# Kernel tuning notes

Measured on AMD Instinct MI355X. Metric: run time of the kernel, lower is better.

Reference implementation:

```python
import jax, jax.numpy as jnp
import numpy as np

B, D, H = 2048, 1024, 16
DH = D // H            # 64 head dim
R = DH // 2            # 32 random-feature dim (kernel_type has no 'northogonal')
EPS = 1e-3             # keras LayerNormalization default epsilon


def _orthogonal(seed):
    # mirrors random_orthogonal(shape=(1,H,1,DH,R)): QR of flat (H*DH, R) matrix
    rng = np.random.default_rng(seed)
    a = rng.standard_normal((H * DH, R)).astype(np.float32)
    q, r = np.linalg.qr(a)
    q = q * np.sign(np.diag(r))[None, :]
    return jnp.asarray(q.reshape(H, DH, R))


def setup_inputs() -> dict:
    key = jax.random.key(0)
    ks = jax.random.split(key, 8)
    inp = {
        "x": jax.random.normal(ks[0], (B, D), jnp.float32),
        # states start as small positive values so den = phi4(q) . new_z > 0
        "s": jax.random.uniform(ks[1], (B, D * R), jnp.float32),
        "z": jax.random.uniform(ks[2], (B, R * H), jnp.float32),
        "ln1_g": jnp.ones((D,), jnp.float32),
        "ln1_b": jnp.zeros((D,), jnp.float32),
        "ln2_g": jnp.ones((D,), jnp.float32),
        "ln2_b": jnp.zeros((D,), jnp.float32),
        "W_attn": jax.random.normal(ks[3], (D, 3 * D), jnp.float32) * 0.02,
        "b_attn": jnp.zeros((3 * D,), jnp.float32),
        "W_proj": jax.random.normal(ks[4], (D, D), jnp.float32) * 0.02,
        "b_proj": jnp.zeros((D,), jnp.float32),
        "W_fc": jax.random.normal(ks[5], (D, 4 * D), jnp.float32) * 0.02,
        "b_fc": jnp.zeros((4 * D,), jnp.float32),
        "W_mp": jax.random.normal(ks[6], (4 * D, D), jnp.float32) * 0.02,
        "b_mp": jnp.zeros((D,), jnp.float32),
    }
    for i in range(4):
        inp[f"w{i + 1}"] = _orthogonal(100 + i)
    return inp


def _ln(x, g, b):
    m = jnp.mean(x, axis=-1, keepdims=True)
    v = jnp.var(x, axis=-1, keepdims=True)
    return g * (x - m) * jax.lax.rsqrt(v + EPS) + b


def _phi(x, w):
    # x: [B,H,dh], w: [H,dh,R] orthogonal random features; kernel 'sigmoid'
    return jax.nn.sigmoid(jnp.einsum('bhd,hdr->bhr', x, w))


def reference(x, s, z, ln1_g, ln1_b, ln2_g, ln2_b, W_attn, b_attn,
              W_proj, b_proj, W_fc, b_fc, W_mp, b_mp, w1, w2, w3, w4):
    bsz = x.shape[0]
    h1 = _ln(x, ln1_g, ln1_b)
    qkv = h1 @ W_attn + b_attn                      # [B, 3D]
    q, k, v = jnp.split(qkv, 3, axis=1)
    q = q.reshape(bsz, H, DH)
    k = k.reshape(bsz, H, DH)
    v = v.reshape(bsz, H, DH)
    s4 = s.reshape(bsz, H, R, DH)
    z3 = z.reshape(bsz, H, R)
    # kernelized linear-attention state update (outer-product accumulation)
    new_s = s4 + jnp.einsum('bhr,bhd->bhrd', _phi(k, w1), v)   # [B,H,R,DH]
    new_z = z3 + _phi(k, w2)                                   # [B,H,R]
    num = jnp.einsum('bhr,bhrd->bhd', _phi(q, w3), new_s)      # [B,H,DH]
    den = jnp.einsum('bhr,bhr->bh', _phi(q, w4), new_z)[..., None]
    head = (num / den).reshape(bsz, D)
    attention = head @ W_proj + b_proj
    h2 = _ln(attention + x, ln2_g, ln2_b)          # dropout: inference mode
    ffn = jax.nn.gelu(h2 @ W_fc + b_fc, approximate=False) @ W_mp + b_mp
    out = h2 + ffn
    return out, new_s.reshape(bsz, D * R), new_z.reshape(bsz, R * H)
```

## Files before the change

### kernel.cpp

```cpp
#include <hip/hip_runtime.h>
#include <hip/hip_bf16.h>
#include <math.h>


#define Bsz 2048
#define Dm  1024
#define Hh  16
#define DHd 64
#define Rr  32

typedef __bf16 bf16x8 __attribute__((ext_vector_type(8)));
typedef float  f32x4  __attribute__((ext_vector_type(4)));

__device__ __forceinline__ float bf2f(__bf16 x) { return (float)x; }
__device__ __forceinline__ __bf16 f2bf(float x) { return (__bf16)x; }

template<bool ADD, typename TA>
__global__ __launch_bounds__(256) void ln_kernel(
    const TA* __restrict__ a, const float* __restrict__ b2,
    const float* __restrict__ g, const float* __restrict__ beta,
    __bf16* __restrict__ outb, float* __restrict__ outf)
{
  const int row = blockIdx.x;
  const int t = threadIdx.x;
  const size_t base = (size_t)row * Dm;
  float vals[4];
#pragma unroll
  for (int i = 0; i < 4; ++i) {
    const int c = t * 4 + i;
    float v = (float)a[base + c];
    if (ADD) v += b2[base + c];
    vals[i] = v;
  }
  float sm = 0.f, sq = 0.f;
#pragma unroll
  for (int i = 0; i < 4; ++i) { sm += vals[i]; sq += vals[i] * vals[i]; }
  for (int off = 32; off > 0; off >>= 1) {
    sm += __shfl_down(sm, off);
    sq += __shfl_down(sq, off);
  }
  __shared__ float smw[4], sqw[4];
  if ((t & 63) == 0) { smw[t >> 6] = sm; sqw[t >> 6] = sq; }
  __syncthreads();
  const float S  = smw[0] + smw[1] + smw[2] + smw[3];
  const float SS = sqw[0] + sqw[1] + sqw[2] + sqw[3];
  const float mean = S * (1.f / Dm);
  const float var  = SS * (1.f / Dm) - mean * mean;
  const float inv  = rsqrtf(var + 1e-3f);
#pragma unroll
  for (int i = 0; i < 4; ++i) {
    const int c = t * 4 + i;
    const float r = g[c] * ((vals[i] - mean) * inv) + beta[c];
    outb[base + c] = f2bf(r);
    if (ADD) outf[base + c] = r;
  }
}

template<bool GELU, bool RES, bool OUTF32>
__global__ __launch_bounds__(256) void gemm_kernel(
    const __bf16* __restrict__ A, const float* __restrict__ B,
    const float* __restrict__ bias, const float* __restrict__ res,
    void* __restrict__ Cv, int M, int N, int K)
{
  __shared__ __align__(16) __bf16 lsA[64][40];
  __shared__ __align__(16) __bf16 lsB[64][40];
  const int t = threadIdx.x;
  const int wave = t >> 6, lane = t & 63;
  const int quad = lane >> 4, l16 = lane & 15;
  const int bm = blockIdx.x * 64, bn = blockIdx.y * 64;
  f32x4 acc0 = {0.f, 0.f, 0.f, 0.f};
  f32x4 acc1 = {0.f, 0.f, 0.f, 0.f};
  f32x4 acc2 = {0.f, 0.f, 0.f, 0.f};
  f32x4 acc3 = {0.f, 0.f, 0.f, 0.f};
  const int arow = t >> 2, acol = (t & 3) * 8;
  const int bncol = t & 63, bkrow = (t >> 6) * 8;
  const size_t abase = (size_t)(bm + arow) * K + acol;

  for (int kt = 0; kt < K; kt += 32) {
    uint4 av = *(const uint4*)(A + abase + kt);
    *(uint4*)(&lsA[arow][acol]) = av;
#pragma unroll
    for (int j = 0; j < 8; ++j)
      lsB[bncol][bkrow + j] = f2bf(B[(size_t)(kt + bkrow + j) * N + bn + bncol]);
    __syncthreads();
    bf16x8 af  = *(const bf16x8*)(&lsA[wave * 16 + l16][quad * 8]);
    bf16x8 bf0 = *(const bf16x8*)(&lsB[      l16][quad * 8]);
    bf16x8 bf1 = *(const bf16x8*)(&lsB[16 + l16][quad * 8]);
    bf16x8 bf2 = *(const bf16x8*)(&lsB[32 + l16][quad * 8]);
    bf16x8 bf3 = *(const bf16x8*)(&lsB[48 + l16][quad * 8]);
    acc0 = __builtin_amdgcn_mfma_f32_16x16x32_bf16(af, bf0, acc0, 0, 0, 0);
    acc1 = __builtin_amdgcn_mfma_f32_16x16x32_bf16(af, bf1, acc1, 0, 0, 0);
    acc2 = __builtin_amdgcn_mfma_f32_16x16x32_bf16(af, bf2, acc2, 0, 0, 0);
    acc3 = __builtin_amdgcn_mfma_f32_16x16x32_bf16(af, bf3, acc3, 0, 0, 0);
    __syncthreads();
  }

  const int m0 = bm + wave * 16 + quad * 4;
  f32x4 accs[4] = {acc0, acc1, acc2, acc3};
#pragma unroll
  for (int ns = 0; ns < 4; ++ns) {
    const int col = bn + ns * 16 + l16;
    const float bv = bias[col];
#pragma unroll
    for (int i = 0; i < 4; ++i) {
      const int row = m0 + i;
      float v = accs[ns][i] + bv;
      if (GELU) v = 0.5f * v * (1.0f + erff(v * 0.70710678118654752f));
      if (RES) v += res[(size_t)row * N + col];
      if (OUTF32) ((float*)Cv)[(size_t)row * N + col] = v;
      else        ((__bf16*)Cv)[(size_t)row * N + col] = f2bf(v);
    }
  }
}

__global__ __launch_bounds__(64) void attn_kernel(
    const float* __restrict__ qkv, const float* __restrict__ s,
    const float* __restrict__ z,
    const float* __restrict__ w1, const float* __restrict__ w2,
    const float* __restrict__ w3, const float* __restrict__ w4,
    float* __restrict__ new_s, float* __restrict__ new_z,
    __bf16* __restrict__ head)
{
  const int bh = blockIdx.x;
  const int b = bh >> 4, h = bh & 15;
  const int tid = threadIdx.x;
  __shared__ float ksh[64], qsh[64];
  __shared__ float phish[4][32];
  __shared__ float nzsh[32];

  const float* qrow = qkv + (size_t)b * (3 * Dm);
  const float qv = qrow[h * 64 + tid];
  const float kv = qrow[Dm + h * 64 + tid];
  const float vv = qrow[2 * Dm + h * 64 + tid];
  qsh[tid] = qv; ksh[tid] = kv;
  __syncthreads();

  {
    const int r = tid & 31;
    const float* wm[4] = {w1, w2, w3, w4};
    for (int mm = (tid >> 5); mm < 4; mm += 2) {
      const float* w = wm[mm] + (size_t)h * (DHd * Rr) + r;
      const float* src = (mm < 2) ? ksh : qsh;
      float acc = 0.f;
#pragma unroll 8
      for (int d = 0; d < 64; ++d) acc += src[d] * w[(size_t)d * 32];
      phish[mm][r] = 1.f / (1.f + expf(-acc));
    }
  }
  __syncthreads();

  const size_t zbase = (size_t)b * (Rr * Hh) + h * Rr;
  if (tid < 32) {
    const float nz = z[zbase + tid] + phish[1][tid];
    new_z[zbase + tid] = nz;
    nzsh[tid] = nz;
  }
  __syncthreads();

  float den = 0.f;
#pragma unroll
  for (int r = 0; r < 32; ++r) den += phish[3][r] * nzsh[r];

  const size_t sbase = ((size_t)b * Hh + h) * (Rr * DHd);
  float num = 0.f;
#pragma unroll 4
  for (int r = 0; r < 32; ++r) {
    const float ns = s[sbase + r * 64 + tid] + phish[0][r] * vv;
    new_s[sbase + r * 64 + tid] = ns;
    num += phish[2][r] * ns;
  }
  head[(size_t)b * Dm + h * 64 + tid] = f2bf(num / den);
}

extern "C" void kernel_launch(void* const* d_in, const int* in_sizes, int n_in,
                              void* d_out, int out_size, void* d_ws, size_t ws_size,
                              hipStream_t stream)
{
  const float* x      = (const float*)d_in[0];
  const float* s_in   = (const float*)d_in[1];
  const float* z_in   = (const float*)d_in[2];
  const float* ln1_g  = (const float*)d_in[3];
  const float* ln1_b  = (const float*)d_in[4];
  const float* ln2_g  = (const float*)d_in[5];
  const float* ln2_b  = (const float*)d_in[6];
  const float* W_attn = (const float*)d_in[7];
  const float* b_attn = (const float*)d_in[8];
  const float* W_proj = (const float*)d_in[9];
  const float* b_proj = (const float*)d_in[10];
  const float* W_fc   = (const float*)d_in[11];
  const float* b_fc   = (const float*)d_in[12];
  const float* W_mp   = (const float*)d_in[13];
  const float* b_mp   = (const float*)d_in[14];
  const float* w1     = (const float*)d_in[15];
  const float* w2     = (const float*)d_in[16];
  const float* w3     = (const float*)d_in[17];
  const float* w4     = (const float*)d_in[18];

  float* out0  = (float*)d_out;
  float* out_s = out0 + (size_t)Bsz * Dm;
  float* out_z = out_s + (size_t)Bsz * Dm * Rr;

  char* ws = (char*)d_ws;
  __bf16* h1    = (__bf16*)ws; ws += (size_t)Bsz * Dm * 2;
  float*  qkv   = (float*) ws; ws += (size_t)Bsz * 3 * Dm * 4;
  __bf16* headp = (__bf16*)ws; ws += (size_t)Bsz * Dm * 2;
  __bf16* attnb = (__bf16*)ws; ws += (size_t)Bsz * Dm * 2;
  __bf16* h2b   = (__bf16*)ws; ws += (size_t)Bsz * Dm * 2;
  float*  h2f   = (float*) ws; ws += (size_t)Bsz * Dm * 4;
  __bf16* fcb   = (__bf16*)ws; ws += (size_t)Bsz * 4 * Dm * 2;

  ln_kernel<false, float><<<Bsz, 256, 0, stream>>>(
      x, nullptr, ln1_g, ln1_b, h1, nullptr);
  gemm_kernel<false, false, true><<<dim3(Bsz / 64, (3 * Dm) / 64), 256, 0, stream>>>(
      h1, W_attn, b_attn, nullptr, qkv, Bsz, 3 * Dm, Dm);
  attn_kernel<<<Bsz * Hh, 64, 0, stream>>>(qkv, s_in, z_in, w1, w2, w3, w4,
                                           out_s, out_z, headp);
  gemm_kernel<false, false, false><<<dim3(Bsz / 64, Dm / 64), 256, 0, stream>>>(
      headp, W_proj, b_proj, nullptr, attnb, Bsz, Dm, Dm);
  ln_kernel<true, __bf16><<<Bsz, 256, 0, stream>>>(
      attnb, x, ln2_g, ln2_b, h2b, h2f);
  gemm_kernel<true, false, false><<<dim3(Bsz / 64, (4 * Dm) / 64), 256, 0, stream>>>(
      h2b, W_fc, b_fc, nullptr, fcb, Bsz, 4 * Dm, Dm);
  gemm_kernel<false, true, true><<<dim3(Bsz / 64, Dm / 64), 256, 0, stream>>>(
      fcb, W_mp, b_mp, h2f, out0, Bsz, Dm, 4 * Dm);
}
```

Before: 803.9 us.

## Pre-transpose weights to bf16 and load GEMM tiles via global_load_lds

Adds a transpose kernel that converts each fp32 weight matrix to a K-contiguous bf16 copy in workspace, run each call. The GEMM then streams both A and B tiles straight into LDS with 16-byte global_load_lds instead of strided scalar fp32 loads plus conversion. Tiles are generalized to BM×BN with a 2x2 wave layout, using 64x128 for the wide QKV and FC GEMMs. Workspace regions are reused by lifetime to fit the weight copies, at the cost of extra transpose launches and traffic on every call.

```diff
diff --git a/kernel.cpp b/kernel.cpp
--- a/kernel.cpp
+++ b/kernel.cpp
@@ -12,8 +12,30 @@
 typedef __bf16 bf16x8 __attribute__((ext_vector_type(8)));
 typedef float  f32x4  __attribute__((ext_vector_type(4)));
 
-__device__ __forceinline__ float bf2f(__bf16 x) { return (float)x; }
 __device__ __forceinline__ __bf16 f2bf(float x) { return (__bf16)x; }
+
+#define GLOAD_LDS16(g, l) __builtin_amdgcn_global_load_lds(               \
+    (const __attribute__((address_space(1))) void*)(g),                   \
+    (__attribute__((address_space(3))) void*)(l), 16, 0, 0)
+
+__global__ __launch_bounds__(256) void wtrans_kernel(
+    const float* __restrict__ W, __bf16* __restrict__ Wt, int K, int N)
+{
+  __shared__ float tile[32][33];
+  const int tx = threadIdx.x & 31;
+  const int ty0 = threadIdx.x >> 5;
+  const int bn = blockIdx.x * 32;
+  const int bk = blockIdx.y * 32;
+#pragma unroll
+  for (int j = 0; j < 4; ++j)
+    tile[ty0 + j * 8][tx] = W[(size_t)(bk + ty0 + j * 8) * N + bn + tx];
+  __syncthreads();
+#pragma unroll
+  for (int j = 0; j < 4; ++j) {
+    const int ny = ty0 + j * 8;
+    Wt[(size_t)(bn + ny) * K + bk + tx] = f2bf(tile[tx][ny]);
+  }
+}
 
 template<bool ADD, typename TA>
 __global__ __launch_bounds__(256) void ln_kernel(
@@ -56,59 +78,74 @@
   }
 }
 
-template<bool GELU, bool RES, bool OUTF32>
+template<int BM, int BN, bool GELU, bool RES, bool OUTF32>
 __global__ __launch_bounds__(256) void gemm_kernel(
-    const __bf16* __restrict__ A, const float* __restrict__ B,
+    const __bf16* __restrict__ A, const __bf16* __restrict__ Bt,
     const float* __restrict__ bias, const float* __restrict__ res,
     void* __restrict__ Cv, int M, int N, int K)
 {
-  __shared__ __align__(16) __bf16 lsA[64][40];
-  __shared__ __align__(16) __bf16 lsB[64][40];
+  constexpr int FM = BM / 32;
+  constexpr int FN = BN / 32;
+  __shared__ __align__(16) __bf16 lsA[BM * 32];
+  __shared__ __align__(16) __bf16 lsB[BN * 32];
   const int t = threadIdx.x;
   const int wave = t >> 6, lane = t & 63;
   const int quad = lane >> 4, l16 = lane & 15;
-  const int bm = blockIdx.x * 64, bn = blockIdx.y * 64;
-  f32x4 acc0 = {0.f, 0.f, 0.f, 0.f};
-  f32x4 acc1 = {0.f, 0.f, 0.f, 0.f};
-  f32x4 acc2 = {0.f, 0.f, 0.f, 0.f};
-  f32x4 acc3 = {0.f, 0.f, 0.f, 0.f};
-  const int arow = t >> 2, acol = (t & 3) * 8;
-  const int bncol = t & 63, bkrow = (t >> 6) * 8;
-  const size_t abase = (size_t)(bm + arow) * K + acol;
+  const int wm = wave >> 1, wn = wave & 1;
+  const int bm = blockIdx.x * BM, bn = blockIdx.y * BN;
+
+  const int srow = lane >> 2, scol = (lane & 3) * 8;
+  const __bf16* Ag  = A  + (size_t)(bm + wave * 16 + srow) * K + scol;
+  const __bf16* Bg0 = Bt + (size_t)(bn + wave * (BN / 4) + srow) * K + scol;
+  const __bf16* Bg1 = Bt + (size_t)(bn + wave * (BN / 4) + 16 + srow) * K + scol;
+  __bf16* lA  = &lsA[wave * 16 * 32];
+  __bf16* lB0 = &lsB[wave * (BN / 4) * 32];
+  __bf16* lB1 = &lsB[(wave * (BN / 4) + 16) * 32];
+
+  f32x4 acc[FM][FN];
+#pragma unroll
+  for (int mi = 0; mi < FM; ++mi)
+#pragma unroll
+    for (int ni = 0; ni < FN; ++ni)
+      acc[mi][ni] = (f32x4){0.f, 0.f, 0.f, 0.f};
 
   for (int kt = 0; kt < K; kt += 32) {
-    uint4 av = *(const uint4*)(A + abase + kt);
-    *(uint4*)(&lsA[arow][acol]) = av;
-#pragma unroll
-    for (int j = 0; j < 8; ++j)
-      lsB[bncol][bkrow + j] = f2bf(B[(size_t)(kt + bkrow + j) * N + bn + bncol]);
+    GLOAD_LDS16(Ag + kt, lA);
+    GLOAD_LDS16(Bg0 + kt, lB0);
+    if constexpr (BN == 128) GLOAD_LDS16(Bg1 + kt, lB1);
     __syncthreads();
-    bf16x8 af  = *(const bf16x8*)(&lsA[wave * 16 + l16][quad * 8]);
-    bf16x8 bf0 = *(const bf16x8*)(&lsB[      l16][quad * 8]);
-    bf16x8 bf1 = *(const bf16x8*)(&lsB[16 + l16][quad * 8]);
-    bf16x8 bf2 = *(const bf16x8*)(&lsB[32 + l16][quad * 8]);
-    bf16x8 bf3 = *(const bf16x8*)(&lsB[48 + l16][quad * 8]);
-    acc0 = __builtin_amdgcn_mfma_f32_16x16x32_bf16(af, bf0, acc0, 0, 0, 0);
-    acc1 = __builtin_amdgcn_mfma_f32_16x16x32_bf16(af, bf1, acc1, 0, 0, 0);
-    acc2 = __builtin_amdgcn_mfma_f32_16x16x32_bf16(af, bf2, acc2, 0, 0, 0);
-    acc3 = __builtin_amdgcn_mfma_f32_16x16x32_bf16(af, bf3, acc3, 0, 0, 0);
+    bf16x8 af[FM], bfr[FN];
+#pragma unroll
+    for (int mi = 0; mi < FM; ++mi)
+      af[mi] = *(const bf16x8*)&lsA[(wm * (BM / 2) + mi * 16 + l16) * 32 + quad * 8];
+#pragma unroll
+    for (int ni = 0; ni < FN; ++ni)
+      bfr[ni] = *(const bf16x8*)&lsB[(wn * (BN / 2) + ni * 16 + l16) * 32 + quad * 8];
+#pragma unroll
+    for (int mi = 0; mi < FM; ++mi)
+#pragma unroll
+      for (int ni = 0; ni < FN; ++ni)
+        acc[mi][ni] = __builtin_amdgcn_mfma_f32_16x16x32_bf16(
+            af[mi], bfr[ni], acc[mi][ni], 0, 0, 0);
     __syncthreads();
   }
 
-  const int m0 = bm + wave * 16 + quad * 4;
-  f32x4 accs[4] = {acc0, acc1, acc2, acc3};
-#pragma unroll
-  for (int ns = 0; ns < 4; ++ns) {
-    const int col = bn + ns * 16 + l16;
-    const float bv = bias[col];
-#pragma unroll
-    for (int i = 0; i < 4; ++i) {
-      const int row = m0 + i;
-      float v = accs[ns][i] + bv;
-      if (GELU) v = 0.5f * v * (1.0f + erff(v * 0.70710678118654752f));
-      if (RES) v += res[(size_t)row * N + col];
-      if (OUTF32) ((float*)Cv)[(size_t)row * N + col] = v;
-      else        ((__bf16*)Cv)[(size_t)row * N + col] = f2bf(v);
+#pragma unroll
+  for (int mi = 0; mi < FM; ++mi) {
+    const int row0 = bm + wm * (BM / 2) + mi * 16 + quad * 4;
+#pragma unroll
+    for (int ni = 0; ni < FN; ++ni) {
+      const int col = bn + wn * (BN / 2) + ni * 16 + l16;
+      const float bv = bias[col];
+#pragma unroll
+      for (int i = 0; i < 4; ++i) {
+        const int row = row0 + i;
+        float v = acc[mi][ni][i] + bv;
+        if (GELU) v = 0.5f * v * (1.0f + erff(v * 0.70710678118654752f));
+        if (RES) v += res[(size_t)row * N + col];
+        if (OUTF32) ((float*)Cv)[(size_t)row * N + col] = v;
+        else        ((__bf16*)Cv)[(size_t)row * N + col] = f2bf(v);
+      }
     }
   }
 }
@@ -201,26 +238,45 @@
   float* out_z = out_s + (size_t)Bsz * Dm * Rr;
 
   char* ws = (char*)d_ws;
-  __bf16* h1    = (__bf16*)ws; ws += (size_t)Bsz * Dm * 2;
-  float*  qkv   = (float*) ws; ws += (size_t)Bsz * 3 * Dm * 4;
-  __bf16* headp = (__bf16*)ws; ws += (size_t)Bsz * Dm * 2;
-  __bf16* attnb = (__bf16*)ws; ws += (size_t)Bsz * Dm * 2;
-  __bf16* h2b   = (__bf16*)ws; ws += (size_t)Bsz * Dm * 2;
-  float*  h2f   = (float*) ws; ws += (size_t)Bsz * Dm * 4;
-  __bf16* fcb   = (__bf16*)ws; ws += (size_t)Bsz * 4 * Dm * 2;
+  __bf16* h1    = (__bf16*)(ws);
+  float*  qkv   = (float*) (ws + ((size_t)4  << 20));
+  __bf16* headp = (__bf16*)(ws + ((size_t)28 << 20));
+  __bf16* attnb = (__bf16*)(ws + ((size_t)32 << 20));
+  __bf16* h2b   = (__bf16*)(ws + ((size_t)36 << 20));
+  float*  h2f   = (float*) (ws + ((size_t)40 << 20));
+  __bf16* fcb   = (__bf16*)(ws + ((size_t)48 << 20));
+  __bf16* Wt_attn = (__bf16*)(ws + ((size_t)48 << 20));
+  __bf16* Wt_proj = (__bf16*)(ws + ((size_t)54 << 20));
+  __bf16* Wt_fc   = (__bf16*)(ws + ((size_t)4  << 20));
+  __bf16* Wt_mp   = (__bf16*)(ws + ((size_t)12 << 20));
+
+  wtrans_kernel<<<dim3((3 * Dm) / 32, Dm / 32), 256, 0, stream>>>(
+      W_attn, Wt_attn, Dm, 3 * Dm);
+  wtrans_kernel<<<dim3(Dm / 32, Dm / 32), 256, 0, stream>>>(
+      W_proj, Wt_proj, Dm, Dm);
 
   ln_kernel<false, float><<<Bsz, 256, 0, stream>>>(
       x, nullptr, ln1_g, ln1_b, h1, nullptr);
-  gemm_kernel<false, false, true><<<dim3(Bsz / 64, (3 * Dm) / 64), 256, 0, stream>>>(
-      h1, W_attn, b_attn, nullptr, qkv, Bsz, 3 * Dm, Dm);
+  gemm_kernel<64, 128, false, false, true>
+      <<<dim3(Bsz / 64, (3 * Dm) / 128), 256, 0, stream>>>(
+      h1, Wt_attn, b_attn, nullptr, qkv, Bsz, 3 * Dm, Dm);
   attn_kernel<<<Bsz * Hh, 64, 0, stream>>>(qkv, s_in, z_in, w1, w2, w3, w4,
                                            out_s, out_z, headp);
-  gemm_kernel<false, false, false><<<dim3(Bsz / 64, Dm / 64), 256, 0, stream>>>(
-      headp, W_proj, b_proj, nullptr, attnb, Bsz, Dm, Dm);
+
+  wtrans_kernel<<<dim3((4 * Dm) / 32, Dm / 32), 256, 0, stream>>>(
+      W_fc, Wt_fc, Dm, 4 * Dm);
+  wtrans_kernel<<<dim3(Dm / 32, (4 * Dm) / 32), 256, 0, stream>>>(
+      W_mp, Wt_mp, 4 * Dm, Dm);
+
+  gemm_kernel<64, 64, false, false, false>
+      <<<dim3(Bsz / 64, Dm / 64), 256, 0, stream>>>(
+      headp, Wt_proj, b_proj, nullptr, attnb, Bsz, Dm, Dm);
   ln_kernel<true, __bf16><<<Bsz, 256, 0, stream>>>(
       attnb, x, ln2_g, ln2_b, h2b, h2f);
-  gemm_kernel<true, false, false><<<dim3(Bsz / 64, (4 * Dm) / 64), 256, 0, stream>>>(
-      h2b, W_fc, b_fc, nullptr, fcb, Bsz, 4 * Dm, Dm);
-  gemm_kernel<false, true, true><<<dim3(Bsz / 64, Dm / 64), 256, 0, stream>>>(
-      fcb, W_mp, b_mp, h2f, out0, Bsz, Dm, 4 * Dm);
-}
+  gemm_kernel<64, 128, true, false, false>
+      <<<dim3(Bsz / 64, (4 * Dm) / 128), 256, 0, stream>>>(
+      h2b, Wt_fc, b_fc, nullptr, fcb, Bsz, 4 * Dm, Dm);
+  gemm_kernel<64, 64, false, true, true>
+      <<<dim3(Bsz / 64, Dm / 64), 256, 0, stream>>>(
+      fcb, Wt_mp, b_mp, h2f, out0, Bsz, Dm, 4 * Dm);
+}
```

New measurement: 701.5 us. 12.7% less time.
